# Kernel optimization log

Hardware: AMD Instinct MI355X
Metric: run time of the kernel (lower is better)

Reference implementation:

```python
import jax, jax.numpy as jnp
import numpy as np
from jax import lax

B, T, H, IN = 2048, 2048, 25, 1


def setup_inputs() -> dict:
    key = jax.random.key(0)
    ks = jax.random.split(key, 7)
    s = 1.0 / np.sqrt(H)  # PyTorch LSTM init scale
    return {
        "x": jax.random.normal(ks[0], (B, T, IN), dtype=jnp.float32),
        "w_ih": jax.random.uniform(ks[1], (4 * H, IN), jnp.float32, -s, s),
        "w_hh": jax.random.uniform(ks[2], (4 * H, H), jnp.float32, -s, s),
        "b_ih": jax.random.uniform(ks[3], (4 * H,), jnp.float32, -s, s),
        "b_hh": jax.random.uniform(ks[4], (4 * H,), jnp.float32, -s, s),
        "w_dense": jax.random.uniform(ks[5], (1, H), jnp.float32, -s, s),
        "b_dense": jax.random.uniform(ks[6], (1,), jnp.float32, -s, s),
    }


def reference(x, w_ih, w_hh, b_ih, b_hh, w_dense, b_dense):
    # x: [B, T, 1] -> scan over time on [T, B, *]
    xt = jnp.swapaxes(x, 0, 1)                     # [T, B, IN]
    x_proj = xt @ w_ih.T + (b_ih + b_hh)           # [T, B, 4H], input projection precomputed

    def step(carry, xp):
        h, c = carry
        gates = xp + h @ w_hh.T                    # [B, 4H]
        i, f, g, o = jnp.split(gates, 4, axis=-1)  # PyTorch gate order i,f,g,o
        i = jax.nn.sigmoid(i)
        f = jax.nn.sigmoid(f)
        g = jnp.tanh(g)
        o = jax.nn.sigmoid(o)
        c = f * c + i * g
        h = o * jnp.tanh(c)
        return (h, c), h

    h0 = jnp.zeros((x.shape[0], H), dtype=x.dtype)
    c0 = jnp.zeros((x.shape[0], H), dtype=x.dtype)
    _, hs = lax.scan(step, (h0, c0), x_proj)       # hs: [T, B, H]
    hs = jnp.swapaxes(hs, 0, 1)                    # [B, T, H]
    return hs @ w_dense.T + b_dense                # [B, T, 1]
```

## Files before the change

### kernel.cpp

```cpp
#include <hip/hip_runtime.h>

#define T_LEN 2048
#define HID   25
#define LOG2E 1.4426950408889634f

typedef float vf4 __attribute__((vector_size(16), may_alias));
typedef float f2  __attribute__((ext_vector_type(2)));

__device__ __forceinline__ float fast_rcp(float x) { return __builtin_amdgcn_rcpf(x); }
__device__ __forceinline__ float fast_exp2(float x) { return __builtin_amdgcn_exp2f(x); }


__global__ __attribute__((amdgpu_flat_work_group_size(256, 256),
                          amdgpu_waves_per_eu(1, 1)))
void lstm_fused(
    const float* __restrict__ x,
    const float* __restrict__ w_ih,
    const float* __restrict__ w_hh,
    const float* __restrict__ b_ih,
    const float* __restrict__ b_hh,
    const float* __restrict__ w_dense,
    const float* __restrict__ b_dense,
    float* __restrict__ out)
{
    const int tid  = threadIdx.x;
    const int u    = tid & 31;
    const int cb   = tid >> 5;
    const int b    = blockIdx.x * 8 + cb;
    const bool act = u < HID;

    __shared__ __align__(16) float hbuf[8][32];
    __shared__ float hist[8][32][33];

    const float si = -LOG2E, sg = 2.f * LOG2E;

    f2 wI2[12], wF2[12], wG2[12], wO2[12];
#pragma unroll
    for (int m = 0; m < 12; ++m) {
        wI2[m] = act ? f2{si * w_hh[u * HID + m],             si * w_hh[u * HID + m + 12]}             : f2{0.f, 0.f};
        wF2[m] = act ? f2{si * w_hh[(HID + u) * HID + m],     si * w_hh[(HID + u) * HID + m + 12]}     : f2{0.f, 0.f};
        wG2[m] = act ? f2{sg * w_hh[(2 * HID + u) * HID + m], sg * w_hh[(2 * HID + u) * HID + m + 12]} : f2{0.f, 0.f};
        wO2[m] = act ? f2{si * w_hh[(3 * HID + u) * HID + m], si * w_hh[(3 * HID + u) * HID + m + 12]} : f2{0.f, 0.f};
    }
    const float wI24 = act ? si * w_hh[u * HID + 24]             : 0.f;
    const float wF24 = act ? si * w_hh[(HID + u) * HID + 24]     : 0.f;
    const float wG24 = act ? sg * w_hh[(2 * HID + u) * HID + 24] : 0.f;
    const float wO24 = act ? si * w_hh[(3 * HID + u) * HID + 24] : 0.f;

    const float bI  = act ? si * (b_ih[u] + b_hh[u]) : 0.f;
    const float bF  = act ? si * (b_ih[HID + u] + b_hh[HID + u]) : 0.f;
    const float bG  = act ? sg * (b_ih[2 * HID + u] + b_hh[2 * HID + u]) : 0.f;
    const float bO  = act ? si * (b_ih[3 * HID + u] + b_hh[3 * HID + u]) : 0.f;
    const float wxI = act ? si * w_ih[u] : 0.f;
    const float wxF = act ? si * w_ih[HID + u] : 0.f;
    const float wxG = act ? sg * w_ih[2 * HID + u] : 0.f;
    const float wxO = act ? si * w_ih[3 * HID + u] : 0.f;
    const float bd  = b_dense[0];

    float wdv[HID];
#pragma unroll
    for (int i = 0; i < HID; ++i) wdv[i] = w_dense[i];

    hbuf[cb][u] = 0.f;

    const int slot = (u < 12) ? 2 * u : (u < 24) ? 2 * u - 23 : u;
    float* hwr = &hbuf[cb][slot];
    const vf4* r4 = (const vf4*)&hbuf[cb][0];
    const float* hbF = &hbuf[cb][0];

    const float4* __restrict__ xp = (const float4*)(x + (size_t)b * T_LEN);
    float* __restrict__ orow = out + (size_t)b * T_LEN;

    f2 hp[12];
#pragma unroll
    for (int m = 0; m < 12; ++m) hp[m] = f2{0.f, 0.f};
    float h24 = 0.f;

    float c = 0.f;
    float4 xcur = xp[0];

    for (int it = 0; it < T_LEN / 4; ++it) {
        const int nx = (it + 1 < T_LEN / 4) ? it + 1 : it;
        float4 xnext = xp[nx];
        float xs[4] = {xcur.x, xcur.y, xcur.z, xcur.w};

#pragma unroll
        for (int s = 0; s < 4; ++s) {
            const float xv = xs[s];
            const int t = 4 * it + s;

            f2 accI = f2{fmaf(xv, wxI, bI), 0.f};
            f2 accF = f2{fmaf(xv, wxF, bF), 0.f};
            f2 accG = f2{fmaf(xv, wxG, bG), 0.f};
            f2 accO = f2{fmaf(xv, wxO, bO), 0.f};
#pragma unroll
            for (int m = 0; m < 12; ++m) {
                const f2 h = hp[m];
                accI = __builtin_elementwise_fma(h, wI2[m], accI);
                accF = __builtin_elementwise_fma(h, wF2[m], accF);
                accG = __builtin_elementwise_fma(h, wG2[m], accG);
                accO = __builtin_elementwise_fma(h, wO2[m], accO);
            }
            const float aI = accI.x + fmaf(h24, wI24, accI.y);
            const float aF = accF.x + fmaf(h24, wF24, accF.y);
            const float aG = accG.x + fmaf(h24, wG24, accG.y);
            const float aO = accO.x + fmaf(h24, wO24, accO.y);

            const float sI = fast_rcp(1.f + fast_exp2(aI));
            const float sF = fast_rcp(1.f + fast_exp2(aF));
            const float sO = fast_rcp(1.f + fast_exp2(aO));
            const float tG = fmaf(-2.f, fast_rcp(1.f + fast_exp2(aG)), 1.f);

            c = fmaf(sF, c, sI * tG);
            const float tC = fmaf(-2.f, fast_rcp(1.f + fast_exp2(2.f * LOG2E * c)), 1.f);
            const float hn = sO * tC;

            *hwr = hn;
            hist[cb][t & 31][u] = hn;
            __asm__ __volatile__("" ::: "memory");
            {
                vf4 a0 = r4[0], a1 = r4[1], a2 = r4[2];
                vf4 a3 = r4[3], a4 = r4[4], a5 = r4[5];
                hp[0]  = f2{a0[0], a0[1]}; hp[1]  = f2{a0[2], a0[3]};
                hp[2]  = f2{a1[0], a1[1]}; hp[3]  = f2{a1[2], a1[3]};
                hp[4]  = f2{a2[0], a2[1]}; hp[5]  = f2{a2[2], a2[3]};
                hp[6]  = f2{a3[0], a3[1]}; hp[7]  = f2{a3[2], a3[3]};
                hp[8]  = f2{a4[0], a4[1]}; hp[9]  = f2{a4[2], a4[3]};
                hp[10] = f2{a5[0], a5[1]}; hp[11] = f2{a5[2], a5[3]};
                h24 = hbF[24];
            }
            __asm__ __volatile__("" ::: "memory");

            if ((t & 31) == 31) {
                const float* hrow = &hist[cb][u][0];
                float ys = 0.f;
#pragma unroll
                for (int i = 0; i < HID; ++i)
                    ys = fmaf(hrow[i], wdv[i], ys);
                orow[(t & ~31) + u] = ys + bd;
            }
        }
        xcur = xnext;
    }
}

extern "C" void kernel_launch(void* const* d_in, const int* in_sizes, int n_in,
                              void* d_out, int out_size, void* d_ws, size_t ws_size,
                              hipStream_t stream) {
    const float* x       = (const float*)d_in[0];
    const float* w_ih    = (const float*)d_in[1];
    const float* w_hh    = (const float*)d_in[2];
    const float* b_ih    = (const float*)d_in[3];
    const float* b_hh    = (const float*)d_in[4];
    const float* w_dense = (const float*)d_in[5];
    const float* b_dense = (const float*)d_in[6];
    float* out = (float*)d_out;

    lstm_fused<<<dim3(256), dim3(256), 0, stream>>>(x, w_ih, w_hh, b_ih, b_hh,
                                                    w_dense, b_dense, out);
}
```

Measured before the change: 546.8 us.

## Split LSTM gates across wave halves, one batch row per wave

Each 64-lane wave now handles one batch element. Lanes 0-31 compute the i and g gates and lanes 32-63 compute the f and o gates, and the i*g product is exchanged across halves with a cross-lane shuffle. This halves per-thread FMA work and register pressure per timestep, which allows 2 waves per EU and doubles the grid to 512 blocks. The cost is a cross-lane shuffle on the serial recurrence path, duplicated c/h computation in both halves, and a larger history buffer.

```diff
diff --git a/kernel.cpp b/kernel.cpp
--- a/kernel.cpp
+++ b/kernel.cpp
@@ -12,7 +12,7 @@
 
 
 __global__ __attribute__((amdgpu_flat_work_group_size(256, 256),
-                          amdgpu_waves_per_eu(1, 1)))
+                          amdgpu_waves_per_eu(2, 2)))
 void lstm_fused(
     const float* __restrict__ x,
     const float* __restrict__ w_ih,
@@ -23,50 +23,50 @@
     const float* __restrict__ b_dense,
     float* __restrict__ out)
 {
-    const int tid  = threadIdx.x;
-    const int u    = tid & 31;
-    const int cb   = tid >> 5;
-    const int b    = blockIdx.x * 8 + cb;
+    const int tid = threadIdx.x;
+    const int l   = tid & 63;
+    const int u   = l & 31;
+    const int hh  = l >> 5;
+    const int w   = tid >> 6;
+    const int b   = blockIdx.x * 4 + w;
     const bool act = u < HID;
 
-    __shared__ __align__(16) float hbuf[8][32];
-    __shared__ float hist[8][32][33];
+    __shared__ __align__(16) float hbuf[4][64];
+    __shared__ float hist[4][64][65];
 
     const float si = -LOG2E, sg = 2.f * LOG2E;
 
-    f2 wI2[12], wF2[12], wG2[12], wO2[12];
+    const int   rowA = hh ? (HID + u)     : u;
+    const int   rowB = hh ? (3 * HID + u) : (2 * HID + u);
+    const float scB  = hh ? si : sg;
+
+    f2 wA2[12], wB2[12];
 #pragma unroll
     for (int m = 0; m < 12; ++m) {
-        wI2[m] = act ? f2{si * w_hh[u * HID + m],             si * w_hh[u * HID + m + 12]}             : f2{0.f, 0.f};
-        wF2[m] = act ? f2{si * w_hh[(HID + u) * HID + m],     si * w_hh[(HID + u) * HID + m + 12]}     : f2{0.f, 0.f};
-        wG2[m] = act ? f2{sg * w_hh[(2 * HID + u) * HID + m], sg * w_hh[(2 * HID + u) * HID + m + 12]} : f2{0.f, 0.f};
-        wO2[m] = act ? f2{si * w_hh[(3 * HID + u) * HID + m], si * w_hh[(3 * HID + u) * HID + m + 12]} : f2{0.f, 0.f};
+        wA2[m] = act ? f2{si  * w_hh[rowA * HID + m], si  * w_hh[rowA * HID + m + 12]} : f2{0.f, 0.f};
+        wB2[m] = act ? f2{scB * w_hh[rowB * HID + m], scB * w_hh[rowB * HID + m + 12]} : f2{0.f, 0.f};
     }
-    const float wI24 = act ? si * w_hh[u * HID + 24]             : 0.f;
-    const float wF24 = act ? si * w_hh[(HID + u) * HID + 24]     : 0.f;
-    const float wG24 = act ? sg * w_hh[(2 * HID + u) * HID + 24] : 0.f;
-    const float wO24 = act ? si * w_hh[(3 * HID + u) * HID + 24] : 0.f;
-
-    const float bI  = act ? si * (b_ih[u] + b_hh[u]) : 0.f;
-    const float bF  = act ? si * (b_ih[HID + u] + b_hh[HID + u]) : 0.f;
-    const float bG  = act ? sg * (b_ih[2 * HID + u] + b_hh[2 * HID + u]) : 0.f;
-    const float bO  = act ? si * (b_ih[3 * HID + u] + b_hh[3 * HID + u]) : 0.f;
-    const float wxI = act ? si * w_ih[u] : 0.f;
-    const float wxF = act ? si * w_ih[HID + u] : 0.f;
-    const float wxG = act ? sg * w_ih[2 * HID + u] : 0.f;
-    const float wxO = act ? si * w_ih[3 * HID + u] : 0.f;
-    const float bd  = b_dense[0];
+    const float wA24 = act ? si  * w_hh[rowA * HID + 24] : 0.f;
+    const float wB24 = act ? scB * w_hh[rowB * HID + 24] : 0.f;
+    const float bA   = act ? si  * (b_ih[rowA] + b_hh[rowA]) : 0.f;
+    const float bB   = act ? scB * (b_ih[rowB] + b_hh[rowB]) : 0.f;
+    const float wxA  = act ? si  * w_ih[rowA] : 0.f;
+    const float wxB  = act ? scB * w_ih[rowB] : 0.f;
+    const float bd   = b_dense[0];
 
     float wdv[HID];
 #pragma unroll
     for (int i = 0; i < HID; ++i) wdv[i] = w_dense[i];
 
-    hbuf[cb][u] = 0.f;
+    hbuf[w][l] = 0.f;
 
-    const int slot = (u < 12) ? 2 * u : (u < 24) ? 2 * u - 23 : u;
-    float* hwr = &hbuf[cb][slot];
-    const vf4* r4 = (const vf4*)&hbuf[cb][0];
-    const float* hbF = &hbuf[cb][0];
+    const int slot = hh ? ((u < 12) ? 2 * u : (u < 24) ? 2 * u - 23 : u)
+                        : (l + 32);
+    float* hwr = &hbuf[w][slot];
+    const vf4* r4 = (const vf4*)&hbuf[w][0];
+    const float* hbF = &hbuf[w][0];
+
+    const int hcol = hh ? u : (32 + l);
 
     const float4* __restrict__ xp = (const float4*)(x + (size_t)b * T_LEN);
     float* __restrict__ orow = out + (size_t)b * T_LEN;
@@ -89,34 +89,30 @@
             const float xv = xs[s];
             const int t = 4 * it + s;
 
-            f2 accI = f2{fmaf(xv, wxI, bI), 0.f};
-            f2 accF = f2{fmaf(xv, wxF, bF), 0.f};
-            f2 accG = f2{fmaf(xv, wxG, bG), 0.f};
-            f2 accO = f2{fmaf(xv, wxO, bO), 0.f};
+            f2 accA = f2{fmaf(xv, wxA, bA), 0.f};
+            f2 accB = f2{fmaf(xv, wxB, bB), 0.f};
 #pragma unroll
             for (int m = 0; m < 12; ++m) {
                 const f2 h = hp[m];
-                accI = __builtin_elementwise_fma(h, wI2[m], accI);
-                accF = __builtin_elementwise_fma(h, wF2[m], accF);
-                accG = __builtin_elementwise_fma(h, wG2[m], accG);
-                accO = __builtin_elementwise_fma(h, wO2[m], accO);
+                accA = __builtin_elementwise_fma(h, wA2[m], accA);
+                accB = __builtin_elementwise_fma(h, wB2[m], accB);
             }
-            const float aI = accI.x + fmaf(h24, wI24, accI.y);
-            const float aF = accF.x + fmaf(h24, wF24, accF.y);
-            const float aG = accG.x + fmaf(h24, wG24, accG.y);
-            const float aO = accO.x + fmaf(h24, wO24, accO.y);
+            const float aA = accA.x + fmaf(h24, wA24, accA.y);
+            const float aB = accB.x + fmaf(h24, wB24, accB.y);
 
-            const float sI = fast_rcp(1.f + fast_exp2(aI));
-            const float sF = fast_rcp(1.f + fast_exp2(aF));
-            const float sO = fast_rcp(1.f + fast_exp2(aO));
-            const float tG = fmaf(-2.f, fast_rcp(1.f + fast_exp2(aG)), 1.f);
+            const float rA = fast_rcp(1.f + fast_exp2(aA));
+            const float rB = fast_rcp(1.f + fast_exp2(aB));
+            const float tB = fmaf(-2.f, rB, 1.f);
 
-            c = fmaf(sF, c, sI * tG);
+            const float p  = rA * tB;
+            const float pX = __shfl_xor(p, 32, 64);
+
+            c = fmaf(rA, c, pX);
             const float tC = fmaf(-2.f, fast_rcp(1.f + fast_exp2(2.f * LOG2E * c)), 1.f);
-            const float hn = sO * tC;
+            const float hn = rB * tC;
 
             *hwr = hn;
-            hist[cb][t & 31][u] = hn;
+            hist[w][t & 63][hcol] = hn;
             __asm__ __volatile__("" ::: "memory");
             {
                 vf4 a0 = r4[0], a1 = r4[1], a2 = r4[2];
@@ -131,13 +127,13 @@
             }
             __asm__ __volatile__("" ::: "memory");
 
-            if ((t & 31) == 31) {
-                const float* hrow = &hist[cb][u][0];
+            if ((t & 63) == 63) {
+                const float* hrow = &hist[w][l][0];
                 float ys = 0.f;
 #pragma unroll
                 for (int i = 0; i < HID; ++i)
                     ys = fmaf(hrow[i], wdv[i], ys);
-                orow[(t & ~31) + u] = ys + bd;
+                orow[(t & ~63) + l] = ys + bd;
             }
         }
         xcur = xnext;
@@ -156,6 +152,6 @@
     const float* b_dense = (const float*)d_in[6];
     float* out = (float*)d_out;
 
-    lstm_fused<<<dim3(256), dim3(256), 0, stream>>>(x, w_ih, w_hh, b_ih, b_hh,
+    lstm_fused<<<dim3(512), dim3(256), 0, stream>>>(x, w_ih, w_hh, b_ih, b_hh,
                                                     w_dense, b_dense, out);
 }
```

New measurement: 587.6 us. 7.5% more time.

## Interleave two independent LSTM batch chains per thread and halve block size

Applied to the files above, without the earlier changes.

Each 64-lane wave now advances two independent pairs of batch recurrences in an interleaved step, instead of one pair per wave. The block shrinks from 256 to 128 threads while covering the same number of batch rows. The goal is to hide the serial latency of the exp/rcp chain and the LDS write-then-read of h behind independent work from the second chain. In exchange, each CU runs half as many waves, so two SIMDs per CU may sit idle. Register pressure also rises because two hidden-state vectors are held at once.

```diff
diff --git a/kernel.cpp b/kernel.cpp
--- a/kernel.cpp
+++ b/kernel.cpp
@@ -11,7 +11,7 @@
 __device__ __forceinline__ float fast_exp2(float x) { return __builtin_amdgcn_exp2f(x); }
 
 
-__global__ __attribute__((amdgpu_flat_work_group_size(256, 256),
+__global__ __attribute__((amdgpu_flat_work_group_size(128, 128),
                           amdgpu_waves_per_eu(1, 1)))
 void lstm_fused(
     const float* __restrict__ x,
@@ -24,13 +24,17 @@
     float* __restrict__ out)
 {
     const int tid  = threadIdx.x;
-    const int u    = tid & 31;
-    const int cb   = tid >> 5;
-    const int b    = blockIdx.x * 8 + cb;
+    const int l    = tid & 63;
+    const int u    = l & 31;
+    const int cbh  = l >> 5;
+    const int w    = tid >> 6;
+    const int base = (blockIdx.x * 2 + w) * 4;
+    const int chP  = base + cbh;
+    const int chQ  = base + 2 + cbh;
     const bool act = u < HID;
 
-    __shared__ __align__(16) float hbuf[8][32];
-    __shared__ float hist[8][32][33];
+    __shared__ __align__(16) float hbuf[2][4][32];
+    __shared__ float hist[2][4][32][33];
 
     const float si = -LOG2E, sg = 2.f * LOG2E;
 
@@ -61,86 +65,103 @@
 #pragma unroll
     for (int i = 0; i < HID; ++i) wdv[i] = w_dense[i];
 
-    hbuf[cb][u] = 0.f;
+    hbuf[w][cbh][u]     = 0.f;
+    hbuf[w][2 + cbh][u] = 0.f;
 
     const int slot = (u < 12) ? 2 * u : (u < 24) ? 2 * u - 23 : u;
-    float* hwr = &hbuf[cb][slot];
-    const vf4* r4 = (const vf4*)&hbuf[cb][0];
-    const float* hbF = &hbuf[cb][0];
+    float* hwrP = &hbuf[w][cbh][slot];
+    float* hwrQ = &hbuf[w][2 + cbh][slot];
+    const vf4* r4P = (const vf4*)&hbuf[w][cbh][0];
+    const vf4* r4Q = (const vf4*)&hbuf[w][2 + cbh][0];
+    const float* hbFP = &hbuf[w][cbh][0];
+    const float* hbFQ = &hbuf[w][2 + cbh][0];
+    float (*histP)[33] = hist[w][cbh];
+    float (*histQ)[33] = hist[w][2 + cbh];
 
-    const float4* __restrict__ xp = (const float4*)(x + (size_t)b * T_LEN);
-    float* __restrict__ orow = out + (size_t)b * T_LEN;
+    const float4* __restrict__ xpP = (const float4*)(x + (size_t)chP * T_LEN);
+    const float4* __restrict__ xpQ = (const float4*)(x + (size_t)chQ * T_LEN);
+    float* __restrict__ orowP = out + (size_t)chP * T_LEN;
+    float* __restrict__ orowQ = out + (size_t)chQ * T_LEN;
 
-    f2 hp[12];
+    f2 hpP[12], hpQ[12];
 #pragma unroll
-    for (int m = 0; m < 12; ++m) hp[m] = f2{0.f, 0.f};
-    float h24 = 0.f;
+    for (int m = 0; m < 12; ++m) { hpP[m] = f2{0.f, 0.f}; hpQ[m] = f2{0.f, 0.f}; }
+    float h24P = 0.f, h24Q = 0.f;
+    float cP = 0.f, cQ = 0.f;
 
-    float c = 0.f;
-    float4 xcur = xp[0];
+    float4 xcP = xpP[0], xcQ = xpQ[0];
+
+    auto step = [&](f2* hp, float& h24, float& c, float xv, int t,
+                    float* hwr, const vf4* r4, const float* hbF,
+                    float (*histc)[33]) {
+        f2 accI = f2{fmaf(xv, wxI, bI), 0.f};
+        f2 accF = f2{fmaf(xv, wxF, bF), 0.f};
+        f2 accG = f2{fmaf(xv, wxG, bG), 0.f};
+        f2 accO = f2{fmaf(xv, wxO, bO), 0.f};
+#pragma unroll
+        for (int m = 0; m < 12; ++m) {
+            const f2 h = hp[m];
+            accI = __builtin_elementwise_fma(h, wI2[m], accI);
+            accF = __builtin_elementwise_fma(h, wF2[m], accF);
+            accG = __builtin_elementwise_fma(h, wG2[m], accG);
+            accO = __builtin_elementwise_fma(h, wO2[m], accO);
+        }
+        const float aI = accI.x + fmaf(h24, wI24, accI.y);
+        const float aF = accF.x + fmaf(h24, wF24, accF.y);
+        const float aG = accG.x + fmaf(h24, wG24, accG.y);
+        const float aO = accO.x + fmaf(h24, wO24, accO.y);
+
+        const float sI = fast_rcp(1.f + fast_exp2(aI));
+        const float sF = fast_rcp(1.f + fast_exp2(aF));
+        const float sO = fast_rcp(1.f + fast_exp2(aO));
+        const float tG = fmaf(-2.f, fast_rcp(1.f + fast_exp2(aG)), 1.f);
+
+        c = fmaf(sF, c, sI * tG);
+        const float tC = fmaf(-2.f, fast_rcp(1.f + fast_exp2(2.f * LOG2E * c)), 1.f);
+        const float hn = sO * tC;
+
+        *hwr = hn;
+        histc[t & 31][u] = hn;
+        {
+            vf4 a0 = r4[0], a1 = r4[1], a2 = r4[2];
+            vf4 a3 = r4[3], a4 = r4[4], a5 = r4[5];
+            hp[0]  = f2{a0[0], a0[1]}; hp[1]  = f2{a0[2], a0[3]};
+            hp[2]  = f2{a1[0], a1[1]}; hp[3]  = f2{a1[2], a1[3]};
+            hp[4]  = f2{a2[0], a2[1]}; hp[5]  = f2{a2[2], a2[3]};
+            hp[6]  = f2{a3[0], a3[1]}; hp[7]  = f2{a3[2], a3[3]};
+            hp[8]  = f2{a4[0], a4[1]}; hp[9]  = f2{a4[2], a4[3]};
+            hp[10] = f2{a5[0], a5[1]}; hp[11] = f2{a5[2], a5[3]};
+            h24 = hbF[24];
+        }
+    };
 
     for (int it = 0; it < T_LEN / 4; ++it) {
         const int nx = (it + 1 < T_LEN / 4) ? it + 1 : it;
-        float4 xnext = xp[nx];
-        float xs[4] = {xcur.x, xcur.y, xcur.z, xcur.w};
+        float4 xnP = xpP[nx], xnQ = xpQ[nx];
+        float xsP[4] = {xcP.x, xcP.y, xcP.z, xcP.w};
+        float xsQ[4] = {xcQ.x, xcQ.y, xcQ.z, xcQ.w};
 
 #pragma unroll
         for (int s = 0; s < 4; ++s) {
-            const float xv = xs[s];
             const int t = 4 * it + s;
-
-            f2 accI = f2{fmaf(xv, wxI, bI), 0.f};
-            f2 accF = f2{fmaf(xv, wxF, bF), 0.f};
-            f2 accG = f2{fmaf(xv, wxG, bG), 0.f};
-            f2 accO = f2{fmaf(xv, wxO, bO), 0.f};
-#pragma unroll
-            for (int m = 0; m < 12; ++m) {
-                const f2 h = hp[m];
-                accI = __builtin_elementwise_fma(h, wI2[m], accI);
-                accF = __builtin_elementwise_fma(h, wF2[m], accF);
-                accG = __builtin_elementwise_fma(h, wG2[m], accG);
-                accO = __builtin_elementwise_fma(h, wO2[m], accO);
-            }
-            const float aI = accI.x + fmaf(h24, wI24, accI.y);
-            const float aF = accF.x + fmaf(h24, wF24, accF.y);
-            const float aG = accG.x + fmaf(h24, wG24, accG.y);
-            const float aO = accO.x + fmaf(h24, wO24, accO.y);
-
-            const float sI = fast_rcp(1.f + fast_exp2(aI));
-            const float sF = fast_rcp(1.f + fast_exp2(aF));
-            const float sO = fast_rcp(1.f + fast_exp2(aO));
-            const float tG = fmaf(-2.f, fast_rcp(1.f + fast_exp2(aG)), 1.f);
-
-            c = fmaf(sF, c, sI * tG);
-            const float tC = fmaf(-2.f, fast_rcp(1.f + fast_exp2(2.f * LOG2E * c)), 1.f);
-            const float hn = sO * tC;
-
-            *hwr = hn;
-            hist[cb][t & 31][u] = hn;
-            __asm__ __volatile__("" ::: "memory");
-            {
-                vf4 a0 = r4[0], a1 = r4[1], a2 = r4[2];
-                vf4 a3 = r4[3], a4 = r4[4], a5 = r4[5];
-                hp[0]  = f2{a0[0], a0[1]}; hp[1]  = f2{a0[2], a0[3]};
-                hp[2]  = f2{a1[0], a1[1]}; hp[3]  = f2{a1[2], a1[3]};
-                hp[4]  = f2{a2[0], a2[1]}; hp[5]  = f2{a2[2], a2[3]};
-                hp[6]  = f2{a3[0], a3[1]}; hp[7]  = f2{a3[2], a3[3]};
-                hp[8]  = f2{a4[0], a4[1]}; hp[9]  = f2{a4[2], a4[3]};
-                hp[10] = f2{a5[0], a5[1]}; hp[11] = f2{a5[2], a5[3]};
-                h24 = hbF[24];
-            }
-            __asm__ __volatile__("" ::: "memory");
+            step(hpP, h24P, cP, xsP[s], t, hwrP, r4P, hbFP, histP);
+            step(hpQ, h24Q, cQ, xsQ[s], t, hwrQ, r4Q, hbFQ, histQ);
 
             if ((t & 31) == 31) {
-                const float* hrow = &hist[cb][u][0];
-                float ys = 0.f;
+                const float* hrP = &histP[u][0];
+                const float* hrQ = &histQ[u][0];
+                float ysP = 0.f, ysQ = 0.f;
 #pragma unroll
-                for (int i = 0; i < HID; ++i)
-                    ys = fmaf(hrow[i], wdv[i], ys);
-                orow[(t & ~31) + u] = ys + bd;
+                for (int i = 0; i < HID; ++i) {
+                    ysP = fmaf(hrP[i], wdv[i], ysP);
+                    ysQ = fmaf(hrQ[i], wdv[i], ysQ);
+                }
+                orowP[(t & ~31) + u] = ysP + bd;
+                orowQ[(t & ~31) + u] = ysQ + bd;
             }
         }
-        xcur = xnext;
+        xcP = xnP;
+        xcQ = xnQ;
     }
 }
 
@@ -156,6 +177,6 @@
     const float* b_dense = (const float*)d_in[6];
     float* out = (float*)d_out;
 
-    lstm_fused<<<dim3(256), dim3(256), 0, stream>>>(x, w_ih, w_hh, b_ih, b_hh,
+    lstm_fused<<<dim3(256), dim3(128), 0, stream>>>(x, w_ih, w_hh, b_ih, b_hh,
                                                     w_dense, b_dense, out);
 }
```

After: 970.5 us. +77.5%, slower.
